# Kernel tuning notes

Measured on AMD Instinct MI355X. Metric: run time of the kernel, lower is better.

The kernel has to match this reference:

```python
import jax, jax.numpy as jnp
import numpy as np

N = 4_000_000   # points at level d
SIDE = 1024     # coordinate range per axis
HALF = SIDE // 2  # parent coord range


def setup_inputs() -> dict:
    key = jax.random.key(0)
    k1, k2 = jax.random.split(key)
    xyz = jax.random.randint(k1, (N, 3), 0, SIDE, dtype=jnp.int32)
    b = (jnp.arange(N, dtype=jnp.int32) % 4)[:, None]  # 4 batches
    coords = jnp.concatenate([b, xyz], axis=1)          # (N,4): [b,x,y,z]
    kernel = jnp.ones((8,), dtype=jnp.float32)          # frozen all-ones 2x2x2 conv weights
    return {"coords": coords, "kernel": kernel}


def _fog(coords, kernel):
    # pos(): occupancy code 2**(x%2 + 2*y%2 + 4*z%2)
    bits = coords[:, 1:4] & 1                       # (N,3)
    off = bits[:, 0] + 2 * bits[:, 1] + 4 * bits[:, 2]  # (N,) child offset in 2x2x2 window
    pos = jnp.exp2(off.astype(jnp.float32))         # (N,) code in {1,2,4,...,128}
    contrib = pos * kernel[off]                     # per-offset conv weight (all ones)
    # stride-2 conv: parent voxel = floor(xyz/2); linearize (b,z,y,x) into a key
    parent = coords[:, 1:4] >> 1                    # (N,3)
    keys = (((coords[:, 0].astype(jnp.int64) * HALF + parent[:, 2]) * HALF
             + parent[:, 1]) * HALF + parent[:, 0])
    ukeys, inv = jnp.unique(keys, return_inverse=True, size=N, fill_value=-1)
    feats = jax.ops.segment_sum(contrib, inv, num_segments=N)[:, None]  # (N,1)
    # decode padded unique keys back to coords; pad slots -> -1
    px = (ukeys % HALF).astype(jnp.int32)
    py = ((ukeys // HALF) % HALF).astype(jnp.int32)
    pz = ((ukeys // (HALF * HALF)) % HALF).astype(jnp.int32)
    pb = (ukeys // (HALF * HALF * HALF)).astype(jnp.int32)
    valid = (ukeys >= 0)[:, None]
    coords_out = jnp.where(valid, jnp.stack([pb, px, py, pz], axis=1), -1)
    return coords_out, feats


def reference(coords, kernel):
    return _fog(coords, kernel)
```

## Files before the change

kernel.cpp:

```cpp
#include <hip/hip_runtime.h>
#include <stdint.h>

typedef unsigned int u32;
typedef unsigned long long u64;

#define LBITS  14
#define LMASK  ((1u << LBITS) - 1u)
#define NBUCK  (1u << (29 - LBITS))
#define BWORDS (1u << (LBITS - 5))
#define WPL    (BWORDS / 64)
#define WOPAD  (BWORDS + BWORDS / 32)
#define FCAP   192
#define BPB    4
#define TILE_A 4096
#define RPT    (TILE_A / 256)
#define CCAP   16384
#define P2T    1024
#define RPT2U  (CCAP / P2T)
#define RECV   4
#define SCAN_ELEM 2048

__device__ __forceinline__ u32 woidx(u32 w) { return w + (w >> 5); }

__device__ __forceinline__ void wsync() {
    asm volatile("s_waitcnt lgkmcnt(0)" ::: "memory");
}

__device__ __forceinline__ u32 make_key(int4 c) {
    return ((((u32)c.x * 512u + ((u32)c.w >> 1)) * 512u + ((u32)c.z >> 1)) * 512u)
           + ((u32)c.y >> 1);
}

__global__ void zero1(u32* __restrict__ p, u32 g) {
    u32 i = blockIdx.x * 256u + threadIdx.x;
    if (i < g) p[i] = 0u;
}

__global__ void __launch_bounds__(256) part1f(const int4* __restrict__ coords,
        u32* __restrict__ ccur, u32* __restrict__ tmp, int n) {
    __shared__ u32 stage[TILE_A];
    __shared__ u32 lcur[256];
    __shared__ u32 gb[256];
    __shared__ u32 wtot[4];
    u32 t = threadIdx.x, wave = t >> 6, lane = t & 63u;
    u32 base = blockIdx.x * TILE_A;
    u32 m = min((u32)TILE_A, (u32)n - base);
    lcur[t] = 0u;
    __syncthreads();
    u32 recv[RPT];
    #pragma unroll
    for (int k = 0; k < RPT; ++k) {
        u32 j = (u32)k * 256u + t;
        if (j < m) {
            int4 c = coords[base + j];
            u32 key = make_key(c);
            u32 off = ((u32)c.y & 1u) | (((u32)c.z & 1u) << 1) | (((u32)c.w & 1u) << 2);
            u32 rec = (key << 3) | off;
            recv[k] = rec;
            atomicAdd(&lcur[rec >> 24], 1u);
        }
    }
    __syncthreads();
    u32 v = lcur[t];
    u32 incl = v;
    #pragma unroll
    for (int d = 1; d < 64; d <<= 1) {
        u32 x = __shfl_up(incl, d);
        if ((int)lane >= d) incl += x;
    }
    if (lane == 63u) wtot[wave] = incl;
    __syncthreads();
    u32 off = (wave > 0u ? wtot[0] : 0u) + (wave > 1u ? wtot[1] : 0u)
            + (wave > 2u ? wtot[2] : 0u);
    u32 excl = off + incl - v;
    u32 gbase = atomicAdd(&ccur[t * 16u], v);
    lcur[t] = excl;
    gb[t] = (t << 14) + gbase - excl;
    __syncthreads();
    #pragma unroll
    for (int k = 0; k < RPT; ++k) {
        u32 j = (u32)k * 256u + t;
        if (j < m) {
            u32 rec = recv[k];
            u32 pos = atomicAdd(&lcur[rec >> 24], 1u);
            stage[pos] = rec;
        }
    }
    __syncthreads();
    for (u32 j = t; j < m; j += 256u) {
        u32 rec = stage[j];
        tmp[gb[rec >> 24] + j] = rec;
    }
}

__global__ void __launch_bounds__(P2T) part2u(u32* __restrict__ tmp,
        const u32* __restrict__ ccur, u32* __restrict__ cstart,
        u32* __restrict__ bcnt, u32* __restrict__ ucount) {
    __shared__ u32 stage[CCAP];
    __shared__ u32 h[4][128];
    __shared__ u32 lstart[128];
    __shared__ u32 lcur[128];
    __shared__ u32 cnts[128];
    __shared__ u32 wtot[2];
    __shared__ u32 bm[16][WOPAD];
    u32 t = threadIdx.x, wave = t >> 6, lane = t & 63u;
    u32 c = blockIdx.x;
    u32 base = c << 14;
    u32 L = ccur[c * 16u];
    if (t < 512u) h[t >> 7][t & 127u] = 0u;
    __syncthreads();
    u32 recv[RPT2U];
    u32 hrep = wave & 3u;
    #pragma unroll
    for (int k = 0; k < RPT2U; ++k) {
        u32 j = (u32)k * P2T + t;
        if (j < L) {
            u32 rec = tmp[base + j];
            recv[k] = rec;
            atomicAdd(&h[hrep][(rec >> 17) & 127u], 1u);
        }
    }
    __syncthreads();
    u32 v = 0, incl = 0;
    if (t < 128u) {
        v = h[0][t] + h[1][t] + h[2][t] + h[3][t];
        incl = v;
        #pragma unroll
        for (int d = 1; d < 64; d <<= 1) {
            u32 x = __shfl_up(incl, d);
            if ((int)lane >= d) incl += x;
        }
        if (lane == 63u) wtot[t >> 6] = incl;
    }
    __syncthreads();
    if (t < 128u) {
        u32 off = (t >= 64u) ? wtot[0] : 0u;
        u32 excl = off + incl - v;
        lstart[t] = excl;
        lcur[t] = excl;
        cnts[t] = v;
        u32 bucket = (c << 7) | t;
        cstart[bucket] = base + excl;
        bcnt[bucket] = v;
    }
    __syncthreads();
    #pragma unroll
    for (int k = 0; k < RPT2U; ++k) {
        u32 j = (u32)k * P2T + t;
        if (j < L) {
            u32 rec = recv[k];
            u32 pos = atomicAdd(&lcur[(rec >> 17) & 127u], 1u);
            stage[pos] = rec;
        }
    }
    __syncthreads();
    for (u32 j = t; j < L; j += P2T) tmp[base + j] = stage[j];
    u32* B = bm[wave];
    for (u32 bi = 0; bi < 8u; ++bi) {
        u32 b = wave * 8u + bi;
        #pragma unroll
        for (int j = 0; j < WPL; ++j) B[woidx(lane * WPL + j)] = 0u;
        wsync();
        u32 s0 = lstart[b], cnt = cnts[b];
        for (u32 i = s0 + lane; i < s0 + cnt; i += 64u) {
            u32 lk = (stage[i] >> 3) & LMASK;
            atomicOr(&B[woidx(lk >> 5)], 1u << (lk & 31u));
        }
        wsync();
        u32 sum = 0;
        #pragma unroll
        for (int j = 0; j < WPL; ++j) sum += __popc(B[woidx(lane * WPL + j)]);
        #pragma unroll
        for (int d = 1; d < 64; d <<= 1) sum += __shfl_xor(sum, d);
        if (lane == 0u) ucount[(c << 7) | b] = sum;
        wsync();
    }
}

__global__ void scan_reduce(const u32* __restrict__ data, u32* __restrict__ partial, u32 G) {
    __shared__ u32 s[256];
    u32 t = threadIdx.x;
    u32 base = blockIdx.x * SCAN_ELEM + t * 8u;
    u32 sum = 0;
    #pragma unroll
    for (int j = 0; j < 8; ++j) { u32 idx = base + j; if (idx < G) sum += data[idx]; }
    s[t] = sum; __syncthreads();
    for (int d = 128; d > 0; d >>= 1) { if ((int)t < d) s[t] += s[t + d]; __syncthreads(); }
    if (t == 0) partial[blockIdx.x] = s[0];
}

__global__ void scan_apply2(const u32* __restrict__ data, u32* __restrict__ out,
                            const u32* __restrict__ partial, u32 G, u32 NB,
                            u32* __restrict__ total) {
    __shared__ u32 s[256];
    __shared__ u32 pb[2];
    u32 t = threadIdx.x;
    u32 p = (t < NB) ? partial[t] : 0u;
    u32 pbef = (t < blockIdx.x) ? p : 0u;
    s[t] = pbef; __syncthreads();
    for (int d = 128; d > 0; d >>= 1) { if ((int)t < d) s[t] += s[t + d]; __syncthreads(); }
    if (t == 0) pb[0] = s[0];
    __syncthreads();
    if (total) {
        s[t] = p; __syncthreads();
        for (int d = 128; d > 0; d >>= 1) { if ((int)t < d) s[t] += s[t + d]; __syncthreads(); }
        if (t == 0) pb[1] = s[0];
        __syncthreads();
        if (blockIdx.x == NB - 1u && t == 0u) total[0] = pb[1];
    }
    u32 base = blockIdx.x * SCAN_ELEM + t * 8u;
    u32 v[8]; u32 sum = 0;
    #pragma unroll
    for (int j = 0; j < 8; ++j) {
        u32 idx = base + j;
        v[j] = (idx < G) ? data[idx] : 0u;
        sum += v[j];
    }
    s[t] = sum; __syncthreads();
    for (int d = 1; d < 256; d <<= 1) {
        u32 add = (t >= (u32)d) ? s[t - d] : 0u;
        __syncthreads(); s[t] += add; __syncthreads();
    }
    u32 run = s[t] - sum + pb[0];
    #pragma unroll
    for (int j = 0; j < 8; ++j) {
        u32 idx = base + j;
        if (idx < G) { u32 x = v[j]; out[idx] = run; run += x; }
    }
}

__global__ void __launch_bounds__(256) pass_emit(const u32* __restrict__ buckrec,
        const u32* __restrict__ cstart, const u32* __restrict__ bcnt,
        const u32* __restrict__ ubase, const float* __restrict__ kern,
        float4* __restrict__ rows, float* __restrict__ feats, int n) {
    __shared__ u32 bm[BPB][WOPAD];
    __shared__ u32 wofW[BPB][BWORDS];
    __shared__ float fl[BPB][FCAP];
    __shared__ float ksc[BPB][8];
    u32 wave = threadIdx.x >> 6, lane = threadIdx.x & 63u;
    u32 bucket = blockIdx.x * BPB + wave;
    u32* B = bm[wave];
    u32* W = wofW[wave];
    float* F = fl[wave];
    #pragma unroll
    for (int j = 0; j < WPL; ++j) B[woidx(lane * WPL + j)] = 0u;
    #pragma unroll
    for (u32 j = lane; j < FCAP; j += 64u) F[j] = 0.f;
    if (lane < 8u) ksc[wave][lane] = (float)(1u << lane) * kern[lane];
    wsync();
    u32 start = cstart[bucket];
    u32 cnt = bcnt[bucket];
    u32 recv[RECV];
    #pragma unroll
    for (int k = 0; k < RECV; ++k) {
        u32 idx = (u32)k * 64u + lane;
        if (idx < cnt) {
            u32 rec = buckrec[start + idx];
            recv[k] = rec;
            u32 lk = (rec >> 3) & LMASK;
            atomicOr(&B[woidx(lk >> 5)], 1u << (lk & 31u));
        }
    }
    wsync();
    u32 wv[WPL]; u32 pc[WPL]; u32 sum = 0;
    #pragma unroll
    for (int j = 0; j < WPL; ++j) {
        wv[j] = B[woidx(lane * WPL + j)];
        pc[j] = __popc(wv[j]);
        sum += pc[j];
    }
    u32 incl = sum;
    #pragma unroll
    for (int d = 1; d < 64; d <<= 1) {
        u32 tt = __shfl_up(incl, d);
        if ((int)lane >= d) incl += tt;
    }
    u32 lex = incl - sum;
    u32 uc = __shfl(incl, 63);
    {
        u32 r = lex;
        #pragma unroll
        for (int j = 0; j < WPL; ++j) { W[((u32)j << 6) | lane] = r; r += pc[j]; }
    }
    wsync();
    u32 base = ubase[bucket];
    bool lds_ok = (uc <= FCAP);
    if (!lds_ok) {
        for (u32 j = lane; j < uc; j += 64u) feats[base + j] = 0.f;
        asm volatile("s_waitcnt vmcnt(0)" ::: "memory");
    }
    #pragma unroll
    for (int k = 0; k < RECV; ++k) {
        u32 idx = (u32)k * 64u + lane;
        if (idx < cnt) {
            u32 rec = recv[k];
            float contrib = ksc[wave][rec & 7u];
            u32 lk = (rec >> 3) & LMASK;
            u32 w = lk >> 5, bit = lk & 31u;
            u32 r = W[((w & 7u) << 6) | (w >> 3)]
                  + __popc(B[woidx(w)] & ((1u << bit) - 1u));
            if (lds_ok) atomicAdd(&F[r], contrib);
            else        atomicAdd(&feats[base + r], contrib);
        }
    }
    wsync();
    u32 rank = base + lex;
    u32 keyhi = bucket << LBITS;
    #pragma unroll
    for (int j = 0; j < WPL; ++j) {
        u32 bits = wv[j];
        u32 kb = keyhi | ((lane * (u32)WPL + (u32)j) << 5);
        while (bits) {
            u32 tz = __builtin_ctz(bits);
            bits &= bits - 1u;
            u32 key = kb | tz;
            rows[rank++] = make_float4((float)(key >> 27), (float)(key & 511u),
                                       (float)((key >> 9) & 511u),
                                       (float)((key >> 18) & 511u));
        }
    }
    if (lds_ok) {
        for (u32 j = lane; j < uc; j += 64u) feats[base + j] = F[j];
    }
}

__global__ void pad_fill(float4* __restrict__ rows, float* __restrict__ feats,
                         const u32* __restrict__ counter, int n) {
    int i = blockIdx.x * blockDim.x + threadIdx.x;
    if (i < n && (u32)i >= counter[0]) {
        rows[i] = make_float4(-1.f, -1.f, -1.f, -1.f);
        feats[i] = 0.f;
    }
}

extern "C" void kernel_launch(void* const* d_in, const int* in_sizes, int n_in,
                              void* d_out, int out_size, void* d_ws, size_t ws_size,
                              hipStream_t stream) {
    const int n = in_sizes[0] / 4;
    const int4* coords = (const int4*)d_in[0];
    const float* kern  = (const float*)d_in[1];
    const u32 NT = ((u32)n + TILE_A - 1) / TILE_A;
    const u32 NB3 = (NBUCK + SCAN_ELEM - 1) / SCAN_ELEM;

    u32* wsp = (u32*)d_ws;
    u32* tmp     = wsp;
    u32* ccur    = tmp + 256 * CCAP;
    u32* cstart  = ccur + 256 * 16;
    u32* bcnt    = cstart + NBUCK;
    u32* ucount  = bcnt + NBUCK;
    u32* ubase   = ucount + NBUCK;
    u32* counter = ubase + NBUCK;
    u32* spart   = counter + 4;

    float4* rows  = (float4*)d_out;
    float*  feats = (float*)((char*)d_out + (size_t)n * 16);

    zero1<<<16, 256, 0, stream>>>(ccur, 256 * 16);
    part1f<<<NT, 256, 0, stream>>>(coords, ccur, tmp, n);
    part2u<<<256, P2T, 0, stream>>>(tmp, ccur, cstart, bcnt, ucount);
    scan_reduce<<<NB3, 256, 0, stream>>>(ucount, spart, NBUCK);
    scan_apply2<<<NB3, 256, 0, stream>>>(ucount, ubase, spart, NBUCK, NB3, counter);
    pass_emit<<<NBUCK / BPB, 256, 0, stream>>>(tmp, cstart, bcnt, ubase, kern,
                                               rows, feats, n);
    pad_fill<<<((u32)n + 255) / 256, 256, 0, stream>>>(rows, feats, counter, n);
}
```

Measured before the change: 206.7 us.

## Fuse bucket scan into part2u/pass_emit and fold pad fill into emit

Replaces the separate scan_reduce/scan_apply2 kernels with a per-chunk exclusive scan inside part2u plus a per-chunk total. Each pass_emit wave then reduces the 256 chunk totals itself to get its global base and the overall unique count. The pad_fill kernel is removed, and padding is spread across emit waves. This cuts three kernel launches and their serial dependencies. The cost is that every wave redundantly reads 256 totals and does the shuffle reductions.

Result: faster. 193.4 us (-6.4%).

```diff
diff --git a/kernel.cpp b/kernel.cpp
--- a/kernel.cpp
+++ b/kernel.cpp
@@ -18,7 +18,6 @@
 #define P2T    1024
 #define RPT2U  (CCAP / P2T)
 #define RECV   4
-#define SCAN_ELEM 2048
 
 __device__ __forceinline__ u32 woidx(u32 w) { return w + (w >> 5); }
 
@@ -95,12 +94,13 @@
 
 __global__ void __launch_bounds__(P2T) part2u(u32* __restrict__ tmp,
         const u32* __restrict__ ccur, u32* __restrict__ cstart,
-        u32* __restrict__ bcnt, u32* __restrict__ ucount) {
+        u32* __restrict__ bcnt, u32* __restrict__ lexc, u32* __restrict__ utot) {
     __shared__ u32 stage[CCAP];
     __shared__ u32 h[4][128];
     __shared__ u32 lstart[128];
     __shared__ u32 lcur[128];
     __shared__ u32 cnts[128];
+    __shared__ u32 ucl[128];
     __shared__ u32 wtot[2];
     __shared__ u32 bm[16][WOPAD];
     u32 t = threadIdx.x, wave = t >> 6, lane = t & 63u;
@@ -172,67 +172,34 @@
         for (int j = 0; j < WPL; ++j) sum += __popc(B[woidx(lane * WPL + j)]);
         #pragma unroll
         for (int d = 1; d < 64; d <<= 1) sum += __shfl_xor(sum, d);
-        if (lane == 0u) ucount[(c << 7) | b] = sum;
+        if (lane == 0u) ucl[b] = sum;
         wsync();
     }
-}
-
-__global__ void scan_reduce(const u32* __restrict__ data, u32* __restrict__ partial, u32 G) {
-    __shared__ u32 s[256];
-    u32 t = threadIdx.x;
-    u32 base = blockIdx.x * SCAN_ELEM + t * 8u;
-    u32 sum = 0;
-    #pragma unroll
-    for (int j = 0; j < 8; ++j) { u32 idx = base + j; if (idx < G) sum += data[idx]; }
-    s[t] = sum; __syncthreads();
-    for (int d = 128; d > 0; d >>= 1) { if ((int)t < d) s[t] += s[t + d]; __syncthreads(); }
-    if (t == 0) partial[blockIdx.x] = s[0];
-}
-
-__global__ void scan_apply2(const u32* __restrict__ data, u32* __restrict__ out,
-                            const u32* __restrict__ partial, u32 G, u32 NB,
-                            u32* __restrict__ total) {
-    __shared__ u32 s[256];
-    __shared__ u32 pb[2];
-    u32 t = threadIdx.x;
-    u32 p = (t < NB) ? partial[t] : 0u;
-    u32 pbef = (t < blockIdx.x) ? p : 0u;
-    s[t] = pbef; __syncthreads();
-    for (int d = 128; d > 0; d >>= 1) { if ((int)t < d) s[t] += s[t + d]; __syncthreads(); }
-    if (t == 0) pb[0] = s[0];
-    __syncthreads();
-    if (total) {
-        s[t] = p; __syncthreads();
-        for (int d = 128; d > 0; d >>= 1) { if ((int)t < d) s[t] += s[t + d]; __syncthreads(); }
-        if (t == 0) pb[1] = s[0];
-        __syncthreads();
-        if (blockIdx.x == NB - 1u && t == 0u) total[0] = pb[1];
-    }
-    u32 base = blockIdx.x * SCAN_ELEM + t * 8u;
-    u32 v[8]; u32 sum = 0;
-    #pragma unroll
-    for (int j = 0; j < 8; ++j) {
-        u32 idx = base + j;
-        v[j] = (idx < G) ? data[idx] : 0u;
-        sum += v[j];
-    }
-    s[t] = sum; __syncthreads();
-    for (int d = 1; d < 256; d <<= 1) {
-        u32 add = (t >= (u32)d) ? s[t - d] : 0u;
-        __syncthreads(); s[t] += add; __syncthreads();
-    }
-    u32 run = s[t] - sum + pb[0];
-    #pragma unroll
-    for (int j = 0; j < 8; ++j) {
-        u32 idx = base + j;
-        if (idx < G) { u32 x = v[j]; out[idx] = run; run += x; }
+    __syncthreads();
+    u32 uv = 0, incl2 = 0;
+    if (t < 128u) {
+        uv = ucl[t];
+        incl2 = uv;
+        #pragma unroll
+        for (int d = 1; d < 64; d <<= 1) {
+            u32 x = __shfl_up(incl2, d);
+            if ((int)lane >= d) incl2 += x;
+        }
+        if (lane == 63u) wtot[t >> 6] = incl2;
+    }
+    __syncthreads();
+    if (t < 128u) {
+        u32 off = (t >= 64u) ? wtot[0] : 0u;
+        lexc[(c << 7) | t] = off + incl2 - uv;
+        if (t == 127u) utot[c] = wtot[0] + incl2;
     }
 }
 
 __global__ void __launch_bounds__(256) pass_emit(const u32* __restrict__ buckrec,
         const u32* __restrict__ cstart, const u32* __restrict__ bcnt,
-        const u32* __restrict__ ubase, const float* __restrict__ kern,
-        float4* __restrict__ rows, float* __restrict__ feats, int n) {
+        const u32* __restrict__ lexc, const u32* __restrict__ utot,
+        const float* __restrict__ kern, float4* __restrict__ rows,
+        float* __restrict__ feats, int n) {
     __shared__ u32 bm[BPB][WOPAD];
     __shared__ u32 wofW[BPB][BWORDS];
     __shared__ float fl[BPB][FCAP];
@@ -261,6 +228,20 @@
             atomicOr(&B[woidx(lk >> 5)], 1u << (lk & 31u));
         }
     }
+    u32 c = bucket >> 7;
+    u32 cb = 0, Uall = 0;
+    #pragma unroll
+    for (int k = 0; k < 4; ++k) {
+        u32 j = (u32)k * 64u + lane;
+        u32 uv = utot[j];
+        Uall += uv;
+        cb += (j < c) ? uv : 0u;
+    }
+    #pragma unroll
+    for (int d = 1; d < 64; d <<= 1) {
+        cb += __shfl_xor(cb, d);
+        Uall += __shfl_xor(Uall, d);
+    }
     wsync();
     u32 wv[WPL]; u32 pc[WPL]; u32 sum = 0;
     #pragma unroll
@@ -283,7 +264,7 @@
         for (int j = 0; j < WPL; ++j) { W[((u32)j << 6) | lane] = r; r += pc[j]; }
     }
     wsync();
-    u32 base = ubase[bucket];
+    u32 base = cb + lexc[bucket];
     bool lds_ok = (uc <= FCAP);
     if (!lds_ok) {
         for (u32 j = lane; j < uc; j += 64u) feats[base + j] = 0.f;
@@ -322,12 +303,11 @@
     if (lds_ok) {
         for (u32 j = lane; j < uc; j += 64u) feats[base + j] = F[j];
     }
-}
-
-__global__ void pad_fill(float4* __restrict__ rows, float* __restrict__ feats,
-                         const u32* __restrict__ counter, int n) {
-    int i = blockIdx.x * blockDim.x + threadIdx.x;
-    if (i < n && (u32)i >= counter[0]) {
+    u32 len = (u32)n - Uall;
+    u32 per = (len + (u32)NBUCK - 1u) / (u32)NBUCK;
+    u32 ps = Uall + bucket * per;
+    u32 pe = min(ps + per, (u32)n);
+    for (u32 i = ps + lane; i < pe; i += 64u) {
         rows[i] = make_float4(-1.f, -1.f, -1.f, -1.f);
         feats[i] = 0.f;
     }
@@ -340,27 +320,21 @@
     const int4* coords = (const int4*)d_in[0];
     const float* kern  = (const float*)d_in[1];
     const u32 NT = ((u32)n + TILE_A - 1) / TILE_A;
-    const u32 NB3 = (NBUCK + SCAN_ELEM - 1) / SCAN_ELEM;
 
     u32* wsp = (u32*)d_ws;
     u32* tmp     = wsp;
     u32* ccur    = tmp + 256 * CCAP;
     u32* cstart  = ccur + 256 * 16;
     u32* bcnt    = cstart + NBUCK;
-    u32* ucount  = bcnt + NBUCK;
-    u32* ubase   = ucount + NBUCK;
-    u32* counter = ubase + NBUCK;
-    u32* spart   = counter + 4;
+    u32* lexc    = bcnt + NBUCK;
+    u32* utot    = lexc + NBUCK;
 
     float4* rows  = (float4*)d_out;
     float*  feats = (float*)((char*)d_out + (size_t)n * 16);
 
     zero1<<<16, 256, 0, stream>>>(ccur, 256 * 16);
     part1f<<<NT, 256, 0, stream>>>(coords, ccur, tmp, n);
-    part2u<<<256, P2T, 0, stream>>>(tmp, ccur, cstart, bcnt, ucount);
-    scan_reduce<<<NB3, 256, 0, stream>>>(ucount, spart, NBUCK);
-    scan_apply2<<<NB3, 256, 0, stream>>>(ucount, ubase, spart, NBUCK, NB3, counter);
-    pass_emit<<<NBUCK / BPB, 256, 0, stream>>>(tmp, cstart, bcnt, ubase, kern,
-                                               rows, feats, n);
-    pad_fill<<<((u32)n + 255) / 256, 256, 0, stream>>>(rows, feats, counter, n);
-}
+    part2u<<<256, P2T, 0, stream>>>(tmp, ccur, cstart, bcnt, lexc, utot);
+    pass_emit<<<NBUCK / BPB, 256, 0, stream>>>(tmp, cstart, bcnt, lexc, utot,
+                                               kern, rows, feats, n);
+}
```
